# Performance work log

Hardware: AMD Instinct MI355X
Metric: run time of the kernel (lower is better)

Reference implementation:

```python
import jax, jax.numpy as jnp
import numpy as np

T = 2048        # flattened tokens (one prefill sequence)
HID = 2048      # hidden_size
NH = 32         # query heads
NKV = 4         # kv heads
HD = 128        # head_dim
THETA = 1000000.0
EPS = 1e-6


def setup_inputs() -> dict:
    key = jax.random.key(0)
    k0, k1, k2 = jax.random.split(key, 3)
    return {
        "positions": jnp.arange(T, dtype=jnp.int32),
        "hidden_states": jax.random.normal(k0, (T, HID), dtype=jnp.float32),
        "w_qkv": jax.random.normal(k1, ((NH + 2 * NKV) * HD, HID), dtype=jnp.float32) * 0.02,
        "w_o": jax.random.normal(k2, (HID, NH * HD), dtype=jnp.float32) * 0.02,
        "q_norm_w": jnp.ones((HD,), dtype=jnp.float32),
        "k_norm_w": jnp.ones((HD,), dtype=jnp.float32),
    }


def _rmsnorm(x, w):
    # per-head RMSNorm over last dim (head_dim), fp32 math
    var = jnp.mean(x * x, axis=-1, keepdims=True)
    return x * jax.lax.rsqrt(var + EPS) * w


def _rope(x, positions):
    # NeoX-style rotary embedding over full head_dim
    d = x.shape[-1]
    inv_freq = 1.0 / (THETA ** (jnp.arange(0, d, 2, dtype=jnp.float32) / d))  # [d/2]
    ang = positions.astype(jnp.float32)[:, None] * inv_freq                   # [T, d/2]
    cos = jnp.cos(ang)[:, None, :]  # [T,1,d/2]
    sin = jnp.sin(ang)[:, None, :]
    x1, x2 = jnp.split(x, 2, axis=-1)
    return jnp.concatenate([x1 * cos - x2 * sin, x2 * cos + x1 * sin], axis=-1)


def reference(positions, hidden_states, w_qkv, w_o, q_norm_w, k_norm_w):
    # fused QKV projection (no bias)
    qkv = hidden_states @ w_qkv.T                       # [T, (NH+2*NKV)*HD]
    q, k, v = jnp.split(qkv, [NH * HD, (NH + NKV) * HD], axis=-1)
    q = _rmsnorm(q.reshape(T, NH, HD), q_norm_w)        # [T,NH,HD]
    k = _rmsnorm(k.reshape(T, NKV, HD), k_norm_w)       # [T,NKV,HD]
    v = v.reshape(T, NKV, HD)
    q = _rope(q, positions)
    k = _rope(k, positions)
    # GQA: expand kv heads to query heads
    g = NH // NKV
    k = jnp.repeat(k, g, axis=1)                        # [T,NH,HD]
    v = jnp.repeat(v, g, axis=1)
    scale = HD ** -0.5
    scores = jnp.einsum('qhd,khd->hqk', q, k) * scale   # [NH,T,T]
    causal = jnp.tril(jnp.ones((T, T), dtype=bool))
    scores = jnp.where(causal[None, :, :], scores, jnp.finfo(scores.dtype).min)
    attn = jax.nn.softmax(scores, axis=-1)
    o = jnp.einsum('hqk,khd->qhd', attn, v).reshape(T, NH * HD)
    return o @ w_o.T                                    # [T,HID]
```

## Files before the change

### kernel.cpp

```cpp
#include <hip/hip_runtime.h>
#include <math.h>

#define T 2048
#define HID 2048
#define NH 32
#define NKV 4
#define HD 128
#define QKV_DIM 5120
#define OD 4096
#define C2LOG 0.12751743f
#define MFIX 6.0f

typedef _Float16 half8 __attribute__((ext_vector_type(8)));
typedef _Float16 half4v __attribute__((ext_vector_type(4)));
typedef float floatx4 __attribute__((ext_vector_type(4)));

#define GLD16(gp, lp) __builtin_amdgcn_global_load_lds( \
    (const __attribute__((address_space(1))) void*)(gp), \
    (__attribute__((address_space(3))) void*)(lp), 16, 0, 0)

__global__ __launch_bounds__(256)
void cvt_all(const float* __restrict__ h, const float* __restrict__ wq,
             const float* __restrict__ wo, _Float16* __restrict__ out) {
    size_t i = ((size_t)blockIdx.x * 256 + threadIdx.x) * 4;
    const float* src;
    size_t off;
    if (i < (size_t)T * HID)                        { src = h;  off = i; }
    else if (i < (size_t)T * HID + (size_t)QKV_DIM * HID)
                                                    { src = wq; off = i - (size_t)T * HID; }
    else                                            { src = wo; off = i - (size_t)T * HID - (size_t)QKV_DIM * HID; }
    float4 v = *(const float4*)(src + off);
    half4v o = { (_Float16)v.x, (_Float16)v.y, (_Float16)v.z, (_Float16)v.w };
    *(half4v*)(out + i) = o;
}

__global__ __launch_bounds__(256)
void gemm_sk_h(const _Float16* __restrict__ A, const _Float16* __restrict__ B,
               _Float16* __restrict__ p0, _Float16* __restrict__ p1,
               int M, int N, int K, int KS) {
    __shared__ __align__(16) _Float16 Asm[8192];
    __shared__ __align__(16) _Float16 Bsm[8192];
    int tid = threadIdx.x;
    int wave = tid >> 6, lane = tid & 63;
    int quad = lane >> 4, l16 = lane & 15;
    int m0 = blockIdx.y * 128, n0 = blockIdx.x * 128;
    int koff = blockIdx.z * KS;
    _Float16* C = blockIdx.z ? p1 : p0;
    int wm = (wave >> 1) * 64, wn = (wave & 1) * 64;
    const _Float16* Ag = A + (size_t)(m0 + (tid >> 2)) * K + koff + (tid & 3) * 8;
    const _Float16* Bg = B + (size_t)(n0 + (tid >> 2)) * K + koff + (tid & 3) * 8;
    size_t row64 = (size_t)64 * K;
    _Float16* AsmW = Asm + wave * 512;
    _Float16* BsmW = Bsm + wave * 512;
    floatx4 acc[4][4] = {};
    for (int k0 = 0; k0 < KS; k0 += 64) {
        __syncthreads();
        GLD16(Ag, AsmW);
        GLD16(Ag + row64, AsmW + 2048);
        GLD16(Ag + 32, AsmW + 4096);
        GLD16(Ag + row64 + 32, AsmW + 6144);
        GLD16(Bg, BsmW);
        GLD16(Bg + row64, BsmW + 2048);
        GLD16(Bg + 32, BsmW + 4096);
        GLD16(Bg + row64 + 32, BsmW + 6144);
        Ag += 64; Bg += 64;
        __syncthreads();
        #pragma unroll
        for (int p = 0; p < 2; p++) {
            half8 af[4], bf[4];
            #pragma unroll
            for (int i = 0; i < 4; i++)
                af[i] = *(const half8*)&Asm[p * 4096 + (wm + i * 16 + l16) * 32 + quad * 8];
            #pragma unroll
            for (int j = 0; j < 4; j++)
                bf[j] = *(const half8*)&Bsm[p * 4096 + (wn + j * 16 + l16) * 32 + quad * 8];
            #pragma unroll
            for (int i = 0; i < 4; i++)
                #pragma unroll
                for (int j = 0; j < 4; j++)
                    acc[i][j] = __builtin_amdgcn_mfma_f32_16x16x32_f16(af[i], bf[j], acc[i][j], 0, 0, 0);
        }
    }
    #pragma unroll
    for (int i = 0; i < 4; i++) {
        int row = m0 + wm + i * 16 + quad * 4;
        #pragma unroll
        for (int j = 0; j < 4; j++) {
            int col = n0 + wn + j * 16 + l16;
            #pragma unroll
            for (int r = 0; r < 4; r++)
                C[(size_t)(row + r) * N + col] = (_Float16)acc[i][j][r];
        }
    }
}

__global__ __launch_bounds__(256)
void gemm_sk_f(const _Float16* __restrict__ A, const _Float16* __restrict__ B,
               _Float16* __restrict__ p0, _Float16* __restrict__ p1,
               _Float16* __restrict__ p2, _Float16* __restrict__ p3,
               int M, int N, int K, int KS) {
    __shared__ __align__(16) _Float16 Asm[8192];
    __shared__ __align__(16) _Float16 Bsm[8192];
    int tid = threadIdx.x;
    int wave = tid >> 6, lane = tid & 63;
    int quad = lane >> 4, l16 = lane & 15;
    int m0 = blockIdx.y * 128, n0 = blockIdx.x * 128;
    int bz = blockIdx.z;
    int koff = bz * KS;
    _Float16* C = (bz == 0) ? p0 : (bz == 1) ? p1 : (bz == 2) ? p2 : p3;
    int wm = (wave >> 1) * 64, wn = (wave & 1) * 64;
    const _Float16* Ag = A + (size_t)(m0 + (tid >> 2)) * K + koff + (tid & 3) * 8;
    const _Float16* Bg = B + (size_t)(n0 + (tid >> 2)) * K + koff + (tid & 3) * 8;
    size_t row64 = (size_t)64 * K;
    _Float16* AsmW = Asm + wave * 512;
    _Float16* BsmW = Bsm + wave * 512;
    floatx4 acc[4][4] = {};
    for (int k0 = 0; k0 < KS; k0 += 64) {
        __syncthreads();
        GLD16(Ag, AsmW);
        GLD16(Ag + row64, AsmW + 2048);
        GLD16(Ag + 32, AsmW + 4096);
        GLD16(Ag + row64 + 32, AsmW + 6144);
        GLD16(Bg, BsmW);
        GLD16(Bg + row64, BsmW + 2048);
        GLD16(Bg + 32, BsmW + 4096);
        GLD16(Bg + row64 + 32, BsmW + 6144);
        Ag += 64; Bg += 64;
        __syncthreads();
        #pragma unroll
        for (int p = 0; p < 2; p++) {
            half8 af[4], bf[4];
            #pragma unroll
            for (int i = 0; i < 4; i++)
                af[i] = *(const half8*)&Asm[p * 4096 + (wm + i * 16 + l16) * 32 + quad * 8];
            #pragma unroll
            for (int j = 0; j < 4; j++)
                bf[j] = *(const half8*)&Bsm[p * 4096 + (wn + j * 16 + l16) * 32 + quad * 8];
            #pragma unroll
            for (int i = 0; i < 4; i++)
                #pragma unroll
                for (int j = 0; j < 4; j++)
                    acc[i][j] = __builtin_amdgcn_mfma_f32_16x16x32_f16(af[i], bf[j], acc[i][j], 0, 0, 0);
        }
    }
    #pragma unroll
    for (int i = 0; i < 4; i++) {
        int row = m0 + wm + i * 16 + quad * 4;
        #pragma unroll
        for (int j = 0; j < 4; j++) {
            int col = n0 + wn + j * 16 + l16;
            #pragma unroll
            for (int r = 0; r < 4; r++)
                C[(size_t)(row + r) * N + col] = (_Float16)acc[i][j][r];
        }
    }
}

__global__ __launch_bounds__(256)
void reduce4(const _Float16* __restrict__ p0, const _Float16* __restrict__ p1,
             const _Float16* __restrict__ p2, const _Float16* __restrict__ p3,
             float* __restrict__ out) {
    size_t i = ((size_t)blockIdx.x * 256 + threadIdx.x) * 4;
    half4v a = *(const half4v*)(p0 + i);
    half4v b = *(const half4v*)(p1 + i);
    half4v c = *(const half4v*)(p2 + i);
    half4v d = *(const half4v*)(p3 + i);
    float4 o = { (float)a.x + (float)b.x + (float)c.x + (float)d.x,
                 (float)a.y + (float)b.y + (float)c.y + (float)d.y,
                 (float)a.z + (float)b.z + (float)c.z + (float)d.z,
                 (float)a.w + (float)b.w + (float)c.w + (float)d.w };
    *(float4*)(out + i) = o;
}

__global__ __launch_bounds__(256)
void qkv_post(const _Float16* __restrict__ qp0, const _Float16* __restrict__ qp1,
              const int* __restrict__ positions,
              const float* __restrict__ qw, const float* __restrict__ kw,
              _Float16* __restrict__ Qb, _Float16* __restrict__ Kb,
              _Float16* __restrict__ Vt) {
    int t = blockIdx.x;
    int wave = threadIdx.x >> 6, lane = threadIdx.x & 63;
    float pos = (float)positions[t];
    float f = exp2f(-(float)lane * (19.9315685693241741f / 64.0f));
    float ang = pos * f;
    float s = sinf(ang), c = cosf(ang);
    const _Float16* r0 = qp0 + (size_t)t * QKV_DIM;
    const _Float16* r1 = qp1 + (size_t)t * QKV_DIM;
    for (int hh = wave; hh < NH + 2 * NKV; hh += 4) {
        float x1 = (float)r0[hh * HD + lane] + (float)r1[hh * HD + lane];
        float x2 = (float)r0[hh * HD + lane + 64] + (float)r1[hh * HD + lane + 64];
        if (hh < NH + NKV) {
            float ss = x1 * x1 + x2 * x2;
            for (int o = 1; o < 64; o <<= 1) ss += __shfl_xor(ss, o);
            float inv = rsqrtf(ss * (1.0f / HD) + 1e-6f);
            const float* w = (hh < NH) ? qw : kw;
            x1 = x1 * inv * w[lane];
            x2 = x2 * inv * w[lane + 64];
            float y1 = x1 * c - x2 * s;
            float y2 = x2 * c + x1 * s;
            _Float16* dst;
            if (hh < NH) dst = Qb + ((size_t)hh * T + t) * HD;
            else         dst = Kb + ((size_t)(hh - NH) * T + t) * HD;
            dst[lane]      = (_Float16)y1;
            dst[lane + 64] = (_Float16)y2;
        } else {
            int hk = hh - NH - NKV;
            Vt[((size_t)hk * HD + lane) * T + t]      = (_Float16)x1;
            Vt[((size_t)hk * HD + lane + 64) * T + t] = (_Float16)x2;
        }
    }
}

__global__ __launch_bounds__(256, 4)
void attn(const _Float16* __restrict__ Qb, const _Float16* __restrict__ Kb,
          const _Float16* __restrict__ Vt, _Float16* __restrict__ Ob) {
    __shared__ __align__(16) _Float16 Ksm[8192];
    __shared__ __align__(16) _Float16 Vsm[8192];
    __shared__ __align__(16) _Float16 Psm[4][1024];
    int b = blockIdx.x;
    int h = b & 31;
    int quarter = b >> 8;
    int i = (b & 255) >> 5;
    int qt = (quarter == 0) ? 31 - i : (quarter == 1) ? i
           : (quarter == 2) ? 23 - i : 8 + i;
    int hk = h >> 3;
    int tid = threadIdx.x, wave = tid >> 6, lane = tid & 63;
    int quad = lane >> 4, l16 = lane & 15;
    int q0 = qt * 64;
    int wbase = q0 + wave * 16;

    half8 aq[4];
    {
        const _Float16* qp = Qb + ((size_t)h * T + wbase + l16) * HD + quad * 8;
        #pragma unroll
        for (int dk = 0; dk < 4; dk++)
            aq[dk] = *(const half8*)(qp + dk * 32);
    }
    floatx4 o_acc[8] = {};
    float lpart[4] = {};

    int krow = tid >> 4;
    const _Float16* Kg = Kb + ((size_t)hk * T + krow) * HD + ((tid & 15) ^ (krow & 7)) * 8;
    int vrow = tid >> 3;
    const _Float16* Vg = Vt + ((size_t)hk * HD + vrow) * T + ((tid & 7) ^ (vrow & 7)) * 8;
    _Float16* KsmW = Ksm + wave * 512;
    _Float16* VsmW = Vsm + wave * 512;
    _Float16* PsmW = Psm[wave];

    int ntiles = qt + 1;
    for (int it = 0; it < ntiles; it++) {
        int kv0 = it * 64;
        __syncthreads();
        {
            const _Float16* kg = Kg + (size_t)kv0 * HD;
            const _Float16* vg = Vg + kv0;
            #pragma unroll
            for (int c = 0; c < 4; c++) {
                GLD16(kg + (size_t)c * (16 * HD), KsmW + c * 2048);
                GLD16(vg + (size_t)c * (32 * T), VsmW + c * 2048);
            }
        }
        __syncthreads();

        floatx4 sfr[4];
        #pragma unroll
        for (int sn = 0; sn < 4; sn++) {
            int row = sn * 16 + l16;
            int rs = row & 7;
            floatx4 a = {};
            #pragma unroll
            for (int dk = 0; dk < 4; dk++) {
                half8 kf = *(const half8*)&Ksm[row * 128 + ((dk * 4 + quad) ^ rs) * 8];
                a = __builtin_amdgcn_mfma_f32_16x16x32_f16(aq[dk], kf, a, 0, 0, 0);
            }
            sfr[sn] = a;
        }

        bool needmask = (it == ntiles - 1);
        int rq = wbase + quad * 4;
        #pragma unroll
        for (int sn = 0; sn < 4; sn++) {
            int kv = kv0 + sn * 16 + l16;
            #pragma unroll
            for (int r = 0; r < 4; r++) {
                float p = __builtin_amdgcn_exp2f(
                    __builtin_fmaf(sfr[sn][r], C2LOG, -MFIX));
                if (needmask) p = (kv <= rq + r) ? p : 0.0f;
                lpart[r] += p;
                int prow = quad * 4 + r;
                int cb = sn * 2 + (l16 >> 3);
                PsmW[prow * 64 + ((cb ^ (prow & 7)) * 8 + (l16 & 7))] = (_Float16)p;
            }
        }
        half8 ap0 = *(const half8*)&PsmW[l16 * 64 + ((quad ^ (l16 & 7)) * 8)];
        half8 ap1 = *(const half8*)&PsmW[l16 * 64 + (((4 + quad) ^ (l16 & 7)) * 8)];

        #pragma unroll
        for (int dn = 0; dn < 8; dn++) {
            int row = dn * 16 + l16;
            int rs = row & 7;
            half8 v0 = *(const half8*)&Vsm[row * 64 + ((quad ^ rs) * 8)];
            half8 v1 = *(const half8*)&Vsm[row * 64 + (((4 + quad) ^ rs) * 8)];
            o_acc[dn] = __builtin_amdgcn_mfma_f32_16x16x32_f16(ap0, v0, o_acc[dn], 0, 0, 0);
            o_acc[dn] = __builtin_amdgcn_mfma_f32_16x16x32_f16(ap1, v1, o_acc[dn], 0, 0, 0);
        }
    }

    #pragma unroll
    for (int o = 1; o < 16; o <<= 1)
        #pragma unroll
        for (int r = 0; r < 4; r++)
            lpart[r] += __shfl_xor(lpart[r], o);
    float linv[4];
    #pragma unroll
    for (int r = 0; r < 4; r++) linv[r] = 1.0f / lpart[r];
    int rowb = wbase + quad * 4;
    #pragma unroll
    for (int dn = 0; dn < 8; dn++) {
        int col = h * HD + dn * 16 + l16;
        #pragma unroll
        for (int r = 0; r < 4; r++)
            Ob[(size_t)(rowb + r) * OD + col] = (_Float16)(o_acc[dn][r] * linv[r]);
    }
}

extern "C" void kernel_launch(void* const* d_in, const int* in_sizes, int n_in,
                              void* d_out, int out_size, void* d_ws, size_t ws_size,
                              hipStream_t stream) {
    const int*   positions = (const int*)d_in[0];
    const float* hidden    = (const float*)d_in[1];
    const float* w_qkv     = (const float*)d_in[2];
    const float* w_o       = (const float*)d_in[3];
    const float* q_norm_w  = (const float*)d_in[4];
    const float* k_norm_w  = (const float*)d_in[5];
    float* out = (float*)d_out;

    const size_t MiB = 1048576;
    char* ws = (char*)d_ws;
    _Float16* hb    = (_Float16*)(ws);
    _Float16* wqkvb = (_Float16*)(ws + 8 * MiB);
    _Float16* wob   = (_Float16*)(ws + 28 * MiB);
    _Float16* qkvp0 = (_Float16*)(ws + 44 * MiB);
    _Float16* qkvp1 = (_Float16*)(ws + 64 * MiB);
    _Float16* Qb    = (_Float16*)(ws + 84 * MiB);
    _Float16* Kb    = (_Float16*)(ws + 100 * MiB);
    _Float16* Vt    = (_Float16*)(ws + 102 * MiB);
    _Float16* Ob    = (_Float16*)(ws + 104 * MiB);
    _Float16* op0   = (_Float16*)(ws);
    _Float16* op1   = (_Float16*)(ws + 9 * MiB);
    _Float16* op2   = (_Float16*)(ws + 44 * MiB);
    _Float16* op3   = (_Float16*)(ws + 53 * MiB);

    cvt_all<<<22528, 256, 0, stream>>>(hidden, w_qkv, w_o, hb);

    gemm_sk_h<<<dim3(QKV_DIM / 128, T / 128, 2), 256, 0, stream>>>(
        hb, wqkvb, qkvp0, qkvp1, T, QKV_DIM, HID, HID / 2);

    qkv_post<<<T, 256, 0, stream>>>(qkvp0, qkvp1, positions, q_norm_w, k_norm_w, Qb, Kb, Vt);

    attn<<<1024, 256, 0, stream>>>(Qb, Kb, Vt, Ob);

    gemm_sk_f<<<dim3(HID / 128, T / 128, 4), 256, 0, stream>>>(
        Ob, wob, op0, op1, op2, op3, T, HID, OD, OD / 4);
    reduce4<<<T * HID / 1024, 256, 0, stream>>>(op0, op1, op2, op3, out);
}
```

Measured before the change: 340.8 us.

## Register-block attention over two query groups per wave with transposed PV output

The attention kernel now runs two waves per block instead of four. Each wave owns 32 query rows split into two 16-row groups, so each K fragment read from LDS feeds MFMAs for both groups. Groups that lie entirely above the causal diagonal for the current tile are skipped. The PV MFMA operands are swapped so the output is transposed, which lets each lane store four contiguous half values, with row sums exchanged through LDS. This trades per-block parallelism and register pressure (double accumulators) for less LDS traffic and wider stores.

```diff
diff --git a/kernel.cpp b/kernel.cpp
--- a/kernel.cpp
+++ b/kernel.cpp
@@ -211,38 +211,39 @@
     }
 }
 
-__global__ __launch_bounds__(256, 4)
+__global__ __launch_bounds__(128)
 void attn(const _Float16* __restrict__ Qb, const _Float16* __restrict__ Kb,
           const _Float16* __restrict__ Vt, _Float16* __restrict__ Ob) {
     __shared__ __align__(16) _Float16 Ksm[8192];
     __shared__ __align__(16) _Float16 Vsm[8192];
-    __shared__ __align__(16) _Float16 Psm[4][1024];
+    __shared__ __align__(16) _Float16 Psm[2][1024];
     int b = blockIdx.x;
     int h = b & 31;
     int quarter = b >> 8;
-    int i = (b & 255) >> 5;
-    int qt = (quarter == 0) ? 31 - i : (quarter == 1) ? i
-           : (quarter == 2) ? 23 - i : 8 + i;
+    int iq = (b & 255) >> 5;
+    int qt = (quarter == 0) ? 31 - iq : (quarter == 1) ? iq
+           : (quarter == 2) ? 23 - iq : 8 + iq;
     int hk = h >> 3;
     int tid = threadIdx.x, wave = tid >> 6, lane = tid & 63;
     int quad = lane >> 4, l16 = lane & 15;
     int q0 = qt * 64;
-    int wbase = q0 + wave * 16;
-
-    half8 aq[4];
-    {
-        const _Float16* qp = Qb + ((size_t)h * T + wbase + l16) * HD + quad * 8;
+    int wbase = q0 + wave * 32;
+
+    half8 aq[2][4];
+    #pragma unroll
+    for (int g = 0; g < 2; g++) {
+        const _Float16* qp = Qb + ((size_t)h * T + wbase + g * 16 + l16) * HD + quad * 8;
         #pragma unroll
         for (int dk = 0; dk < 4; dk++)
-            aq[dk] = *(const half8*)(qp + dk * 32);
-    }
-    floatx4 o_acc[8] = {};
-    float lpart[4] = {};
-
-    int krow = tid >> 4;
-    const _Float16* Kg = Kb + ((size_t)hk * T + krow) * HD + ((tid & 15) ^ (krow & 7)) * 8;
-    int vrow = tid >> 3;
-    const _Float16* Vg = Vt + ((size_t)hk * HD + vrow) * T + ((tid & 7) ^ (vrow & 7)) * 8;
+            aq[g][dk] = *(const half8*)(qp + dk * 32);
+    }
+    floatx4 o_acc[2][8] = {};
+    float lpart[2][4] = {};
+
+    int krow = wave * 4 + (lane >> 4);
+    const _Float16* Kg = Kb + ((size_t)hk * T + krow) * HD + ((lane & 15) ^ (krow & 7)) * 8;
+    int vrow = wave * 8 + (lane >> 3);
+    const _Float16* Vg = Vt + ((size_t)hk * HD + vrow) * T + ((lane & 7) ^ (vrow & 7)) * 8;
     _Float16* KsmW = Ksm + wave * 512;
     _Float16* VsmW = Vsm + wave * 512;
     _Float16* PsmW = Psm[wave];
@@ -255,45 +256,61 @@
             const _Float16* kg = Kg + (size_t)kv0 * HD;
             const _Float16* vg = Vg + kv0;
             #pragma unroll
-            for (int c = 0; c < 4; c++) {
-                GLD16(kg + (size_t)c * (16 * HD), KsmW + c * 2048);
-                GLD16(vg + (size_t)c * (32 * T), VsmW + c * 2048);
+            for (int c = 0; c < 8; c++) {
+                GLD16(kg + (size_t)c * (8 * HD), KsmW + c * 1024);
+                GLD16(vg + (size_t)c * (16 * T), VsmW + c * 1024);
             }
         }
         __syncthreads();
 
-        floatx4 sfr[4];
+        bool act[2];
+        act[0] = (kv0 <= wbase + 15);
+        act[1] = (kv0 <= wbase + 31);
+
+        floatx4 sfr[2][4];
         #pragma unroll
         for (int sn = 0; sn < 4; sn++) {
             int row = sn * 16 + l16;
             int rs = row & 7;
-            floatx4 a = {};
-            #pragma unroll
-            for (int dk = 0; dk < 4; dk++) {
-                half8 kf = *(const half8*)&Ksm[row * 128 + ((dk * 4 + quad) ^ rs) * 8];
-                a = __builtin_amdgcn_mfma_f32_16x16x32_f16(aq[dk], kf, a, 0, 0, 0);
+            half8 kf[4];
+            #pragma unroll
+            for (int dk = 0; dk < 4; dk++)
+                kf[dk] = *(const half8*)&Ksm[row * 128 + ((dk * 4 + quad) ^ rs) * 8];
+            #pragma unroll
+            for (int g = 0; g < 2; g++) {
+                if (!act[g]) continue;
+                floatx4 a = {};
+                #pragma unroll
+                for (int dk = 0; dk < 4; dk++)
+                    a = __builtin_amdgcn_mfma_f32_16x16x32_f16(aq[g][dk], kf[dk], a, 0, 0, 0);
+                sfr[g][sn] = a;
             }
-            sfr[sn] = a;
-        }
-
-        bool needmask = (it == ntiles - 1);
-        int rq = wbase + quad * 4;
-        #pragma unroll
-        for (int sn = 0; sn < 4; sn++) {
-            int kv = kv0 + sn * 16 + l16;
-            #pragma unroll
-            for (int r = 0; r < 4; r++) {
-                float p = __builtin_amdgcn_exp2f(
-                    __builtin_fmaf(sfr[sn][r], C2LOG, -MFIX));
-                if (needmask) p = (kv <= rq + r) ? p : 0.0f;
-                lpart[r] += p;
-                int prow = quad * 4 + r;
-                int cb = sn * 2 + (l16 >> 3);
-                PsmW[prow * 64 + ((cb ^ (prow & 7)) * 8 + (l16 & 7))] = (_Float16)p;
+        }
+
+        half8 ap[2][2];
+        #pragma unroll
+        for (int g = 0; g < 2; g++) {
+            if (!act[g]) continue;
+            int bg = wbase + g * 16;
+            bool needmask = (kv0 + 63 > bg);
+            int rq = bg + quad * 4;
+            #pragma unroll
+            for (int sn = 0; sn < 4; sn++) {
+                int kv = kv0 + sn * 16 + l16;
+                #pragma unroll
+                for (int r = 0; r < 4; r++) {
+                    float p = __builtin_amdgcn_exp2f(
+                        __builtin_fmaf(sfr[g][sn][r], C2LOG, -MFIX));
+                    if (needmask) p = (kv <= rq + r) ? p : 0.0f;
+                    lpart[g][r] += p;
+                    int prow = quad * 4 + r;
+                    int cb = sn * 2 + (l16 >> 3);
+                    PsmW[prow * 64 + ((cb ^ (prow & 7)) * 8 + (l16 & 7))] = (_Float16)p;
+                }
             }
-        }
-        half8 ap0 = *(const half8*)&PsmW[l16 * 64 + ((quad ^ (l16 & 7)) * 8)];
-        half8 ap1 = *(const half8*)&PsmW[l16 * 64 + (((4 + quad) ^ (l16 & 7)) * 8)];
+            ap[g][0] = *(const half8*)&PsmW[l16 * 64 + ((quad ^ (l16 & 7)) * 8)];
+            ap[g][1] = *(const half8*)&PsmW[l16 * 64 + (((4 + quad) ^ (l16 & 7)) * 8)];
+        }
 
         #pragma unroll
         for (int dn = 0; dn < 8; dn++) {
@@ -301,26 +318,42 @@
             int rs = row & 7;
             half8 v0 = *(const half8*)&Vsm[row * 64 + ((quad ^ rs) * 8)];
             half8 v1 = *(const half8*)&Vsm[row * 64 + (((4 + quad) ^ rs) * 8)];
-            o_acc[dn] = __builtin_amdgcn_mfma_f32_16x16x32_f16(ap0, v0, o_acc[dn], 0, 0, 0);
-            o_acc[dn] = __builtin_amdgcn_mfma_f32_16x16x32_f16(ap1, v1, o_acc[dn], 0, 0, 0);
-        }
-    }
-
-    #pragma unroll
-    for (int o = 1; o < 16; o <<= 1)
-        #pragma unroll
-        for (int r = 0; r < 4; r++)
-            lpart[r] += __shfl_xor(lpart[r], o);
-    float linv[4];
-    #pragma unroll
-    for (int r = 0; r < 4; r++) linv[r] = 1.0f / lpart[r];
-    int rowb = wbase + quad * 4;
-    #pragma unroll
-    for (int dn = 0; dn < 8; dn++) {
-        int col = h * HD + dn * 16 + l16;
-        #pragma unroll
-        for (int r = 0; r < 4; r++)
-            Ob[(size_t)(rowb + r) * OD + col] = (_Float16)(o_acc[dn][r] * linv[r]);
+            #pragma unroll
+            for (int g = 0; g < 2; g++) {
+                if (!act[g]) continue;
+                o_acc[g][dn] = __builtin_amdgcn_mfma_f32_16x16x32_f16(v0, ap[g][0], o_acc[g][dn], 0, 0, 0);
+                o_acc[g][dn] = __builtin_amdgcn_mfma_f32_16x16x32_f16(v1, ap[g][1], o_acc[g][dn], 0, 0, 0);
+            }
+        }
+    }
+
+    #pragma unroll
+    for (int g = 0; g < 2; g++)
+        #pragma unroll
+        for (int o = 1; o < 16; o <<= 1)
+            #pragma unroll
+            for (int r = 0; r < 4; r++)
+                lpart[g][r] += __shfl_xor(lpart[g][r], o);
+    float* Lsm = (float*)PsmW;
+    if (l16 == 0) {
+        #pragma unroll
+        for (int g = 0; g < 2; g++)
+            #pragma unroll
+            for (int r = 0; r < 4; r++)
+                Lsm[g * 16 + quad * 4 + r] = lpart[g][r];
+    }
+    #pragma unroll
+    for (int g = 0; g < 2; g++) {
+        float linv = 1.0f / Lsm[g * 16 + l16];
+        int trow = wbase + g * 16 + l16;
+        #pragma unroll
+        for (int dn = 0; dn < 8; dn++) {
+            half4v st = { (_Float16)(o_acc[g][dn][0] * linv),
+                          (_Float16)(o_acc[g][dn][1] * linv),
+                          (_Float16)(o_acc[g][dn][2] * linv),
+                          (_Float16)(o_acc[g][dn][3] * linv) };
+            *(half4v*)(Ob + (size_t)trow * OD + h * HD + dn * 16 + quad * 4) = st;
+        }
     }
 }
 
@@ -358,7 +391,7 @@
 
     qkv_post<<<T, 256, 0, stream>>>(qkvp0, qkvp1, positions, q_norm_w, k_norm_w, Qb, Kb, Vt);
 
-    attn<<<1024, 256, 0, stream>>>(Qb, Kb, Vt, Ob);
+    attn<<<1024, 128, 0, stream>>>(Qb, Kb, Vt, Ob);
 
     gemm_sk_f<<<dim3(HID / 128, T / 128, 4), 256, 0, stream>>>(
         Ob, wob, op0, op1, op2, op3, T, HID, OD, OD / 4);
```

Result: slower. 353.3 us (+3.7%).
